# Kernel optimization log

Hardware: AMD Instinct MI355X
Metric: run time of the kernel (lower is better)

The kernel has to match this reference:

```python
import jax, jax.numpy as jnp
import numpy as np

B, S, IN, D, H, L, T, C = 64, 448, 128, 512, 8, 6, 3, 3
FF = 6 * D
MAXLEN = 500
PH = 4  # pooling heads


def _ln(x, w, b, eps=1e-5):
    m = x.mean(-1, keepdims=True)
    v = ((x - m) ** 2).mean(-1, keepdims=True)
    return (x - m) / jnp.sqrt(v + eps) * w + b


def _gelu(x):
    return jax.nn.gelu(x, approximate=False)


def setup_inputs():
    key = jax.random.key(0)
    ks = iter(jax.random.split(key, 64))
    p = lambda *sh: jax.random.normal(next(ks), sh, jnp.float32) * 0.02
    z = lambda *sh: jnp.zeros(sh, jnp.float32)
    o = lambda *sh: jnp.ones(sh, jnp.float32)
    return dict(
        x=jax.random.normal(next(ks), (B, S, IN), jnp.float32),
        in_w1=p(IN, D // 2), in_b1=z(D // 2), in_w2=p(D // 2, D), in_b2=z(D),
        in_ln_w=o(D), in_ln_b=z(D), pos=p(MAXLEN, D), cls=p(1, 1, D),
        wq=p(L, D, D), bq=z(L, D), wk=p(L, D, D), bk=z(L, D),
        wv=p(L, D, D), bv=z(L, D), wo=p(L, D, D), bo=z(L, D),
        conv_w=p(L, D, 1, 3), conv_b=z(L, D), aln_w=o(L, D), aln_b=z(L, D),
        f_w1=p(L, D, FF), f_b1=z(L, FF), f_w2=p(L, FF, FF), f_b2=z(L, FF),
        f_w3=p(L, FF, D), f_b3=z(L, D), g_w=p(L, D, D), g_b=z(L, D),
        n1_w=o(L, D), n1_b=z(L, D), n2_w=o(L, D), n2_b=z(L, D),
        pq=p(1, 1, D), pqw=p(D, D), pqb=z(D), pkw=p(D, D), pkb=z(D),
        pvw=p(D, D), pvb=z(D), pow_w=p(D, D), pow_b=z(D),
        pln_w=o(D), pln_b=z(D),
        h_ln_w=o(T, 2 * D), h_ln_b=z(T, 2 * D),
        h_w1=p(T, 2 * D, 2 * D), h_b1=z(T, 2 * D),
        h_w2=p(T, 2 * D, D), h_b2=z(T, D),
        h_w3=p(T, D, D // 2), h_b3=z(T, D // 2),
        h_w4=p(T, D // 2, C), h_b4=z(T, C),
        u_w1=p(T, 2 * D, D // 2), u_b1=z(T, D // 2),
        u_w2=p(T, D // 2, 1), u_b2=z(T, 1),
    )


def _forward(x, in_w1, in_b1, in_w2, in_b2, in_ln_w, in_ln_b, pos, cls,
             wq, bq, wk, bk, wv, bv, wo, bo, conv_w, conv_b, aln_w, aln_b,
             f_w1, f_b1, f_w2, f_b2, f_w3, f_b3, g_w, g_b,
             n1_w, n1_b, n2_w, n2_b,
             pq, pqw, pqb, pkw, pkb, pvw, pvb, pow_w, pow_b, pln_w, pln_b,
             h_ln_w, h_ln_b, h_w1, h_b1, h_w2, h_b2, h_w3, h_b3, h_w4, h_b4,
             u_w1, u_b1, u_w2, u_b2):
    b = x.shape[0]
    # input projection + norm + pos + cls token
    h = _gelu(x @ in_w1 + in_b1) @ in_w2 + in_b2
    h = _ln(h, in_ln_w, in_ln_b)
    h = h + pos[: h.shape[1]][None]
    h = jnp.concatenate([jnp.broadcast_to(cls, (b, 1, D)), h], axis=1)
    S1 = h.shape[1]  # S + 1
    dk = D // H
    for i in range(L):
        # multi-scale attention (dropout off in eval)
        q = (h @ wq[i] + bq[i]).reshape(b, S1, H, dk)
        k = (h @ wk[i] + bk[i]).reshape(b, S1, H, dk)
        v = (h @ wv[i] + bv[i]).reshape(b, S1, H, dk)
        attn = jax.nn.softmax(jnp.einsum('bqhd,bkhd->bhqk', q, k) / np.sqrt(dk), axis=-1)
        ga = jnp.einsum('bhqk,bkhd->bqhd', attn, v).reshape(b, S1, D) @ wo[i] + bo[i]
        # parallel depthwise conv branch (kernel=3, groups=D)
        la = jax.lax.conv_general_dilated(
            h.transpose(0, 2, 1), conv_w[i], (1,), [(1, 1)],
            dimension_numbers=('NCH', 'OIH', 'NCH'), feature_group_count=D)
        la = (la + conv_b[i][None, :, None]).transpose(0, 2, 1)
        attn_out = _ln(h + (ga + 0.3 * la), aln_w[i], aln_b[i])
        h = _ln(h + attn_out, n1_w[i], n1_b[i])
        # gated FFN
        f = _gelu(h @ f_w1[i] + f_b1[i])
        f = _gelu(f @ f_w2[i] + f_b2[i])
        f = f @ f_w3[i] + f_b3[i]
        gate = jax.nn.sigmoid(h @ g_w[i] + g_b[i])
        h = _ln(h + f * gate, n2_w[i], n2_b[i])
    cls_out = h[:, 0]
    xs = h[:, 1:]
    # attention pooling (torch MHA with 4 heads, single learned query)
    pdk = D // PH
    q = (jnp.broadcast_to(pq, (b, 1, D)) @ pqw + pqb).reshape(b, 1, PH, pdk)
    k = (xs @ pkw + pkb).reshape(b, -1, PH, pdk)
    v = (xs @ pvw + pvb).reshape(b, -1, PH, pdk)
    a = jax.nn.softmax(jnp.einsum('bqhd,bkhd->bhqk', q, k) / np.sqrt(pdk), axis=-1)
    po = jnp.einsum('bhqk,bkhd->bqhd', a, v).reshape(b, 1, D) @ pow_w + pow_b
    pooled = _ln(po[:, 0], pln_w, pln_b)
    comb = jnp.concatenate([cls_out, pooled], axis=-1)  # (B, 2D)
    logits, unc = [], []
    for t in range(T):
        hh = _ln(comb, h_ln_w[t], h_ln_b[t])
        hh = _gelu(hh @ h_w1[t] + h_b1[t])
        hh = _gelu(hh @ h_w2[t] + h_b2[t])
        hh = _gelu(hh @ h_w3[t] + h_b3[t])
        logits.append(hh @ h_w4[t] + h_b4[t])
        uu = jax.nn.relu(comb @ u_w1[t] + u_b1[t]) @ u_w2[t] + u_b2[t]
        unc.append(jax.nn.softplus(uu[:, 0]))
    return jnp.stack(logits, 1), jnp.stack(unc, 1)


def reference(x, in_w1, in_b1, in_w2, in_b2, in_ln_w, in_ln_b, pos, cls,
              wq, bq, wk, bk, wv, bv, wo, bo, conv_w, conv_b, aln_w, aln_b,
              f_w1, f_b1, f_w2, f_b2, f_w3, f_b3, g_w, g_b,
              n1_w, n1_b, n2_w, n2_b,
              pq, pqw, pqb, pkw, pkb, pvw, pvb, pow_w, pow_b, pln_w, pln_b,
              h_ln_w, h_ln_b, h_w1, h_b1, h_w2, h_b2, h_w3, h_b3, h_w4, h_b4,
              u_w1, u_b1, u_w2, u_b2):
    return _forward(x, in_w1, in_b1, in_w2, in_b2, in_ln_w, in_ln_b, pos, cls,
                    wq, bq, wk, bk, wv, bv, wo, bo, conv_w, conv_b, aln_w, aln_b,
                    f_w1, f_b1, f_w2, f_b2, f_w3, f_b3, g_w, g_b,
                    n1_w, n1_b, n2_w, n2_b,
                    pq, pqw, pqb, pkw, pkb, pvw, pvb, pow_w, pow_b, pln_w, pln_b,
                    h_ln_w, h_ln_b, h_w1, h_b1, h_w2, h_b2, h_w3, h_b3, h_w4, h_b4,
                    u_w1, u_b1, u_w2, u_b2)
```

## Files before the change

### kernel.cpp

```cpp
#include <hip/hip_runtime.h>

#define BB 64
#define SS 448
#define S1 449
#define DD 512
#define HH 8
#define LL 6
#define TT 3
#define FF 3072
#define NS 28672
#define N1 28736
#define N1P 28800
#define FBROWS 3712

typedef unsigned short u16;
typedef __attribute__((ext_vector_type(8))) short short8;
typedef __attribute__((ext_vector_type(4))) float floatx4;

#define AS1C(p) ((const __attribute__((address_space(1))) void*)(p))
#define AS3P(p) ((__attribute__((address_space(3))) void*)(p))

__device__ __forceinline__ float b2f(u16 u){
  union { float f; unsigned u; } x; x.u = ((unsigned)u) << 16; return x.f;
}
__device__ __forceinline__ u16 f2b(float f){
  union { float f; unsigned u; } x; x.f = f;
  unsigned r = x.u + 0x7FFFu + ((x.u >> 16) & 1u);
  return (u16)(r >> 16);
}
__device__ __forceinline__ float gelu_f(float v){ return 0.5f*v*(1.f+erff(v*0.70710678118654752440f)); }
__device__ __forceinline__ float sigm_f(float v){ return 1.f/(1.f+expf(-v)); }

__device__ __forceinline__ void reduce2(float& a, float& b, float* scr){
  #pragma unroll
  for (int off=1; off<64; off<<=1){ a += __shfl_xor(a, off); b += __shfl_xor(b, off); }
  const int w = threadIdx.x >> 6;
  __syncthreads();
  if ((threadIdx.x & 63) == 0){ scr[w] = a; scr[4+w] = b; }
  __syncthreads();
  a = scr[0]+scr[1]+scr[2]+scr[3];
  b = scr[4]+scr[5]+scr[6]+scr[7];
}

__global__ void transcvt(const float* __restrict__ src, u16* __restrict__ dst, int K, int N){
  __shared__ float t[32][33];
  const size_t bo = (size_t)blockIdx.z * K * N;
  src += bo; dst += bo;
  const int k0 = blockIdx.x*32, n0 = blockIdx.y*32;
  const int tx = threadIdx.x, ty = threadIdx.y;
  #pragma unroll
  for (int i=0;i<32;i+=8) t[ty+i][tx] = src[(size_t)(k0+ty+i)*N + n0+tx];
  __syncthreads();
  #pragma unroll
  for (int i=0;i<32;i+=8) dst[(size_t)(n0+ty+i)*K + k0+tx] = f2b(t[tx][ty+i]);
}

__global__ void cvt(const float* __restrict__ src, u16* __restrict__ dst, int n){
  int i = blockIdx.x*256 + threadIdx.x;
  if (i < n) dst[i] = f2b(src[i]);
}

template<int ACT, int HASMUL>
__launch_bounds__(256)
__global__ void gemm128(const u16* __restrict__ A, int lda,
                        const u16* __restrict__ Bt, int ldb,
                        const float* __restrict__ bias,
                        u16* __restrict__ Cp, int ldc,
                        const u16* __restrict__ mulp,
                        int K)
{
  __shared__ u16 Al[4096];
  __shared__ u16 Bl[4096];
  const int tid = threadIdx.x;
  const int lane = tid & 63;
  const int w = tid >> 6;
  const int wm = (w >> 1) * 64;
  const int wn = (w & 1) * 64;
  const size_t m0 = (size_t)blockIdx.x * 128;
  const size_t n0 = (size_t)blockIdx.y * 128;

  const int c1 = 256 + tid;
  const u16* a0 = A + (m0 + (tid>>2))*lda + (tid&3)*8;
  const u16* a1 = A + (m0 + (c1>>2))*lda + (c1&3)*8;
  const u16* b0 = Bt + (n0 + (tid>>2))*ldb + (tid&3)*8;
  const u16* b1 = Bt + (n0 + (c1>>2))*ldb + (c1&3)*8;

  const floatx4 fz = {0.f,0.f,0.f,0.f};
  floatx4 acc[4][4];
  #pragma unroll
  for (int i=0;i<4;i++)
    #pragma unroll
    for (int j=0;j<4;j++) acc[i][j] = fz;

  const int fr = lane & 15;
  const int fq = (lane >> 4) * 8;

  for (int k0 = 0; k0 < K; k0 += 32) {
    __syncthreads();
    __builtin_amdgcn_global_load_lds(AS1C(a0), AS3P(Al + w*512),        16, 0, 0);
    __builtin_amdgcn_global_load_lds(AS1C(a1), AS3P(Al + 2048 + w*512), 16, 0, 0);
    __builtin_amdgcn_global_load_lds(AS1C(b0), AS3P(Bl + w*512),        16, 0, 0);
    __builtin_amdgcn_global_load_lds(AS1C(b1), AS3P(Bl + 2048 + w*512), 16, 0, 0);
    a0 += 32; a1 += 32; b0 += 32; b1 += 32;
    __syncthreads();
    short8 af[4], bf[4];
    #pragma unroll
    for (int i=0;i<4;i++) af[i] = *(const short8*)(Al + (wm + i*16 + fr)*32 + fq);
    #pragma unroll
    for (int j=0;j<4;j++) bf[j] = *(const short8*)(Bl + (wn + j*16 + fr)*32 + fq);
    #pragma unroll
    for (int i=0;i<4;i++)
      #pragma unroll
      for (int j=0;j<4;j++)
        acc[i][j] = __builtin_amdgcn_mfma_f32_16x16x32_bf16(af[i], bf[j], acc[i][j], 0, 0, 0);
  }

  const int cr = (lane >> 4) * 4;
  const int cc = lane & 15;
  #pragma unroll
  for (int i=0;i<4;i++) {
    #pragma unroll
    for (int j=0;j<4;j++) {
      const size_t gc = n0 + wn + j*16 + cc;
      const float bv = bias[gc];
      #pragma unroll
      for (int r=0;r<4;r++) {
        const size_t gr = m0 + wm + i*16 + cr + r;
        float vv = acc[i][j][r] + bv;
        if (ACT==1) vv = gelu_f(vv);
        if (ACT==2) vv = sigm_f(vv);
        if (HASMUL) vv *= b2f(mulp[gr*ldc + gc]);
        Cp[gr*ldc + gc] = f2b(vv);
      }
    }
  }
}

__launch_bounds__(256)
__global__ void flash_attn(const u16* __restrict__ qg, const u16* __restrict__ kg,
                           const u16* __restrict__ vg, u16* __restrict__ ctx)
{
  const int bid = blockIdx.x;
  const int qt = bid & 7;
  const int h  = (bid >> 3) & 7;
  const int b  = bid >> 6;
  const int tid = threadIdx.x;
  const int lane = tid & 63;
  const int w = tid >> 6;

  __shared__ u16 Kl[32*64];
  __shared__ u16 Vt[64*72];
  __shared__ u16 Pl[4][16*32];

  const int fr = lane & 15;
  const int fq = (lane >> 4) * 8;

  const int qrow = qt*64 + w*16;
  const size_t qoff = ((size_t)b*S1 + qrow + fr)*DD + h*64 + fq;
  const short8 qf0 = *(const short8*)(qg + qoff);
  const short8 qf1 = *(const short8*)(qg + qoff + 32);

  const floatx4 fz = {0.f,0.f,0.f,0.f};
  floatx4 oacc[4] = {fz, fz, fz, fz};
  float mm[4] = {-3e30f,-3e30f,-3e30f,-3e30f};
  float ll[4] = {0.f,0.f,0.f,0.f};

  const int key_t = tid >> 3;
  const int kch  = tid & 7;
  const u16* gk_base = kg + ((size_t)b*S1 + key_t)*DD + h*64 + kch*8;
  const u16* gv_base = vg + ((size_t)b*S1 + key_t)*DD + h*64 + kch*8;

  for (int k0 = 0; k0 < 480; k0 += 32) {
    __syncthreads();
    __builtin_amdgcn_global_load_lds(AS1C(gk_base + (size_t)k0*DD), AS3P(Kl + w*512), 16, 0, 0);
    {
      short8 tv = *(const short8*)(gv_base + (size_t)k0*DD);
      #pragma unroll
      for (int i=0;i<8;i++) Vt[(kch*8+i)*72 + key_t] = (u16)tv[i];
    }
    __syncthreads();

    floatx4 s0 = fz, s1 = fz;
    {
      short8 kb0  = *(const short8*)(Kl + (size_t)fr*64 + fq);
      short8 kb0h = *(const short8*)(Kl + (size_t)fr*64 + 32 + fq);
      s0 = __builtin_amdgcn_mfma_f32_16x16x32_bf16(qf0, kb0,  s0, 0,0,0);
      s0 = __builtin_amdgcn_mfma_f32_16x16x32_bf16(qf1, kb0h, s0, 0,0,0);
      short8 kb1  = *(const short8*)(Kl + (size_t)(16+fr)*64 + fq);
      short8 kb1h = *(const short8*)(Kl + (size_t)(16+fr)*64 + 32 + fq);
      s1 = __builtin_amdgcn_mfma_f32_16x16x32_bf16(qf0, kb1,  s1, 0,0,0);
      s1 = __builtin_amdgcn_mfma_f32_16x16x32_bf16(qf1, kb1h, s1, 0,0,0);
    }
    const bool msk0 = (k0 + fr) >= S1;
    const bool msk1 = (k0 + 16 + fr) >= S1;
    float p0[4], p1[4];
    #pragma unroll
    for (int r=0;r<4;r++) {
      p0[r] = msk0 ? -3e30f : s0[r]*0.125f;
      p1[r] = msk1 ? -3e30f : s1[r]*0.125f;
    }
    #pragma unroll
    for (int r=0;r<4;r++) {
      float t = fmaxf(p0[r], p1[r]);
      t = fmaxf(t, __shfl_xor(t,1)); t = fmaxf(t, __shfl_xor(t,2));
      t = fmaxf(t, __shfl_xor(t,4)); t = fmaxf(t, __shfl_xor(t,8));
      float mn = fmaxf(mm[r], t);
      float al = __expf(mm[r]-mn);
      mm[r] = mn;
      float e0 = msk0 ? 0.f : __expf(p0[r]-mn);
      float e1 = msk1 ? 0.f : __expf(p1[r]-mn);
      p0[r]=e0; p1[r]=e1;
      float rs = e0+e1;
      rs += __shfl_xor(rs,1); rs += __shfl_xor(rs,2);
      rs += __shfl_xor(rs,4); rs += __shfl_xor(rs,8);
      ll[r] = ll[r]*al + rs;
      oacc[0][r]*=al; oacc[1][r]*=al; oacc[2][r]*=al; oacc[3][r]*=al;
    }
    const int pr = (lane>>4)*4;
    #pragma unroll
    for (int r=0;r<4;r++) {
      Pl[w][(pr+r)*32 + fr]      = f2b(p0[r]);
      Pl[w][(pr+r)*32 + 16 + fr] = f2b(p1[r]);
    }
    short8 pf = *(const short8*)(&Pl[w][fr*32 + fq]);
    #pragma unroll
    for (int j=0;j<4;j++) {
      short8 vb = *(const short8*)(Vt + (size_t)(j*16+fr)*72 + fq);
      oacc[j] = __builtin_amdgcn_mfma_f32_16x16x32_bf16(pf, vb, oacc[j], 0,0,0);
    }
  }
  const int pr = (lane>>4)*4;
  #pragma unroll
  for (int r=0;r<4;r++) {
    const int qi = qrow + pr + r;
    if (qi < S1) {
      const size_t base = ((size_t)b*S1 + qi)*DD + h*64 + fr;
      const float inv = 1.f/ll[r];
      ctx[base]    = f2b(oacc[0][r]*inv);
      ctx[base+16] = f2b(oacc[1][r]*inv);
      ctx[base+32] = f2b(oacc[2][r]*inv);
      ctx[base+48] = f2b(oacc[3][r]*inv);
    }
  }
}

__global__ void ln_pos_cls(const u16* __restrict__ t2, const float* __restrict__ lw,
                           const float* __restrict__ lb, const float* __restrict__ pos,
                           const float* __restrict__ cls, u16* __restrict__ h16)
{
  __shared__ float scr[8];
  const int row = blockIdx.x;
  const int b = row / S1, s = row % S1;
  const int tid = threadIdx.x;
  if (s == 0) {
// ... 111 lines not shown
  __syncthreads();
  mx = fmaxf(fmaxf(scr[0],scr[1]), fmaxf(scr[2],scr[3]));
  float ps = 0.f;
  #pragma unroll
  for (int it=0;it<2;it++){
    const int key = tid+it*256;
    if (key<448) { float p = __expf(s[it]-mx); sc[key]=p; ps += p; }
  }
  #pragma unroll
  for (int off=1; off<64; off<<=1) ps += __shfl_xor(ps, off);
  __syncthreads();
  if ((tid&63)==0) scr[4+w] = ps;
  __syncthreads();
  const float lsum = scr[4]+scr[5]+scr[6]+scr[7];
  const int d = tid & 127, half = tid >> 7;
  float acc = 0.f;
  for (int key = half*224; key < half*224+224; key++)
    acc += sc[key] * b2f(vp[((size_t)b*SS+key)*DD + ph*128 + d]);
  red[tid] = acc;
  __syncthreads();
  if (tid < 128) po[(size_t)b*DD + ph*128 + tid] = f2b((red[tid]+red[tid+128])/lsum);
}

__global__ void comb_build(const u16* __restrict__ hfin, const float* __restrict__ po2,
                           const float* __restrict__ plw, const float* __restrict__ plb,
                           float* __restrict__ c32, u16* __restrict__ c16)
{
  __shared__ float scr[8];
  const int b = blockIdx.x, tid = threadIdx.x;
  #pragma unroll
  for (int e=0;e<2;e++) {
    const int d = tid+e*256;
    const float v = b2f(hfin[((size_t)b*S1)*DD + d]);
    c32[(size_t)b*1024+d] = v; c16[(size_t)b*1024+d] = f2b(v);
  }
  const float* x = po2 + (size_t)b*DD;
  float v0=x[tid], v1=x[tid+256];
  float sa=v0+v1, sb=v0*v0+v1*v1;
  reduce2(sa,sb,scr);
  float mean=sa*(1.f/512.f), var=sb*(1.f/512.f)-mean*mean;
  float inv=rsqrtf(var+1e-5f);
  float r0=(v0-mean)*inv*plw[tid]+plb[tid];
  float r1=(v1-mean)*inv*plw[tid+256]+plb[tid+256];
  c32[(size_t)b*1024+512+tid]=r0; c32[(size_t)b*1024+512+tid+256]=r1;
  c16[(size_t)b*1024+512+tid]=f2b(r0); c16[(size_t)b*1024+512+tid+256]=f2b(r1);
}

__global__ void head_ln(const float* __restrict__ c32, const float* __restrict__ lw,
                        const float* __restrict__ lb, u16* __restrict__ out)
{
  __shared__ float scr[8];
  const int r = blockIdx.x;
  const int t = r / 64, b = r % 64;
  const int tid = threadIdx.x;
  const float* x = c32 + (size_t)b*1024;
  float v[4]; float sa=0.f, sb=0.f;
  #pragma unroll
  for (int e=0;e<4;e++){ v[e]=x[tid+e*256]; sa+=v[e]; sb+=v[e]*v[e]; }
  reduce2(sa,sb,scr);
  float mean=sa*(1.f/1024.f), var=sb*(1.f/1024.f)-mean*mean;
  float inv=rsqrtf(var+1e-5f);
  #pragma unroll
  for (int e=0;e<4;e++){
    const int d = tid+e*256;
    out[(size_t)r*1024+d] = f2b((v[e]-mean)*inv*lw[t*1024+d] + lb[t*1024+d]);
  }
}

template<int ACT, int OUTBF>
__launch_bounds__(256)
__global__ void wavedot(const u16* __restrict__ A, int K, int aMod,
                        const u16* __restrict__ Wt,
                        const float* __restrict__ bias,
                        void* __restrict__ out, int N, int rows, int rowsPerT)
{
  const int gw = (int)(((size_t)blockIdx.x*256 + threadIdx.x) >> 6);
  const int lane = threadIdx.x & 63;
  if (gw >= rows*N) return;
  const int row = gw / N, col = gw % N;
  const int t = row / rowsPerT;
  const int arow = row % aMod;
  const u16* a  = A + (size_t)arow*K;
  const u16* wv = Wt + ((size_t)t*N + col)*K;
  float acc = 0.f;
  for (int k = lane*8; k < K; k += 512) {
    short8 a8 = *(const short8*)(a+k);
    short8 w8 = *(const short8*)(wv+k);
    #pragma unroll
    for (int i=0;i<8;i++) acc += b2f((u16)a8[i]) * b2f((u16)w8[i]);
  }
  #pragma unroll
  for (int off=1; off<64; off<<=1) acc += __shfl_xor(acc, off);
  if (lane == 0) {
    float v = acc + bias[t*N + col];
    if (ACT==1) v = gelu_f(v);
    if (ACT==2) v = fmaxf(v, 0.f);
    if (OUTBF) ((u16*)out)[(size_t)row*N+col] = f2b(v);
    else       ((float*)out)[(size_t)row*N+col] = v;
  }
}

__global__ void logits_k(const float* __restrict__ hh3, const float* __restrict__ w4,
                         const float* __restrict__ b4, float* __restrict__ out)
{
  const int e = blockIdx.x*256 + threadIdx.x;
  if (e >= 576) return;
  const int t = e / 192;
  const int rem = e % 192;
  const int b = rem / 3, c = rem % 3;
  const float* a = hh3 + (size_t)(t*64 + b)*256;
  const float* w = w4 + (size_t)t*256*3 + c;
  float acc = b4[t*3+c];
  for (int k=0;k<256;k++) acc += a[k]*w[k*3];
  out[(size_t)(b*3 + t)*3 + c] = acc;
}

__global__ void u2_k(const float* __restrict__ uu, const float* __restrict__ w2,
                     const float* __restrict__ b2, float* __restrict__ out)
{
  const int e = blockIdx.x*256 + threadIdx.x;
  if (e >= 192) return;
  const int t = e / 64, b = e % 64;
  const float* a = uu + (size_t)e*256;
  const float* w = w2 + (size_t)t*256;
  float acc = b2[t];
  for (int k=0;k<256;k++) acc += a[k]*w[k];
  acc = (acc > 30.f) ? acc : log1pf(expf(acc));
  out[576 + b*3 + t] = acc;
}

extern "C" void kernel_launch(void* const* d_in, const int* in_sizes, int n_in,
                              void* d_out, int out_size, void* d_ws, size_t ws_size,
                              hipStream_t stream)
{
  const float* x      = (const float*)d_in[0];
  const float* in_w1  = (const float*)d_in[1];
  const float* in_b1  = (const float*)d_in[2];
  const float* in_w2  = (const float*)d_in[3];
  const float* in_b2  = (const float*)d_in[4];
  const float* in_lnw = (const float*)d_in[5];
  const float* in_lnb = (const float*)d_in[6];
  const float* pos    = (const float*)d_in[7];
  const float* cls    = (const float*)d_in[8];
  const float* wq     = (const float*)d_in[9];
  const float* bq     = (const float*)d_in[10];
  const float* wk     = (const float*)d_in[11];
  const float* bk     = (const float*)d_in[12];
  const float* wv     = (const float*)d_in[13];
  const float* bv     = (const float*)d_in[14];
// ... 32 lines not shown
  const float* h_b1   = (const float*)d_in[47];
  const float* h_w2   = (const float*)d_in[48];
  const float* h_b2   = (const float*)d_in[49];
  const float* h_w3   = (const float*)d_in[50];
  const float* h_b3   = (const float*)d_in[51];
  const float* h_w4   = (const float*)d_in[52];
  const float* h_b4   = (const float*)d_in[53];
  const float* u_w1   = (const float*)d_in[54];
  const float* u_b1   = (const float*)d_in[55];
  const float* u_w2   = (const float*)d_in[56];
  const float* u_b2   = (const float*)d_in[57];
  float* out = (float*)d_out;

  char* wsp = (char*)d_ws;
  size_t off = 0;
  auto alloc = [&](size_t bytes) -> char* {
    char* p = wsp + off;
    off += (bytes + 255) & ~(size_t)255;
    return p;
  };

  u16* w_in1T = (u16*)alloc((size_t)256*128*2);
  u16* w_in2T = (u16*)alloc((size_t)512*256*2);
  u16* wqT  = (u16*)alloc((size_t)LL*512*512*2);
  u16* wkT  = (u16*)alloc((size_t)LL*512*512*2);
  u16* wvT  = (u16*)alloc((size_t)LL*512*512*2);
  u16* woT  = (u16*)alloc((size_t)LL*512*512*2);
  u16* gwT  = (u16*)alloc((size_t)LL*512*512*2);
  u16* fw1T = (u16*)alloc((size_t)3072*512*2);
  u16* fw2T = (u16*)alloc((size_t)3072*3072*2);
  u16* fw3T = (u16*)alloc((size_t)512*3072*2);
  u16* pkwT = (u16*)alloc((size_t)512*512*2);
  u16* pvwT = (u16*)alloc((size_t)512*512*2);
  u16* powT = (u16*)alloc((size_t)512*512*2);
  u16* pqwT = (u16*)alloc((size_t)512*512*2);
  u16* hw1T = (u16*)alloc((size_t)TT*1024*1024*2);
  u16* hw2T = (u16*)alloc((size_t)TT*512*1024*2);
  u16* hw3T = (u16*)alloc((size_t)TT*256*512*2);
  u16* uw1T = (u16*)alloc((size_t)TT*256*1024*2);

  u16* hA16 = (u16*)alloc((size_t)N1P*DD*2);
  u16* hB16 = (u16*)alloc((size_t)N1P*DD*2);
  u16* q16  = (u16*)alloc((size_t)N1P*DD*2);
  u16* k16  = (u16*)alloc((size_t)N1P*DD*2);
  u16* v16  = (u16*)alloc((size_t)N1P*DD*2);
  u16* fbuf1 = (u16*)alloc((size_t)FBROWS*FF*2);
  u16* fbuf2 = (u16*)alloc((size_t)FBROWS*FF*2);
  u16* ctx16  = hB16;
  u16* tmpa16 = k16;
  u16* gate16 = q16;
  u16* x16 = fbuf1;
  u16* t1b = fbuf2;
  u16* pq16   = (u16*)alloc(512*2);
  float* qvec = (float*)alloc(512*4);
  u16* po16   = (u16*)alloc((size_t)64*512*2);
  float* po2  = (float*)alloc((size_t)64*512*4);
  float* comb32 = (float*)alloc((size_t)64*1024*4);
  u16*   comb16 = (u16*)alloc((size_t)64*1024*2);
  u16* hh0 = (u16*)alloc((size_t)192*1024*2);
  u16* hh1 = (u16*)alloc((size_t)192*1024*2);
  u16* hh2 = (u16*)alloc((size_t)192*512*2);
  float* hh3 = (float*)alloc((size_t)192*256*4);
  float* uu  = (float*)alloc((size_t)192*256*4);
  (void)ws_size;

  const dim3 tb(32,8);
  transcvt<<<dim3(4,8,1),   tb, 0, stream>>>(in_w1, w_in1T, 128, 256);
  transcvt<<<dim3(8,16,1),  tb, 0, stream>>>(in_w2, w_in2T, 256, 512);
  transcvt<<<dim3(16,16,LL),tb, 0, stream>>>(wq,  wqT, 512, 512);
  transcvt<<<dim3(16,16,LL),tb, 0, stream>>>(wk,  wkT, 512, 512);
  transcvt<<<dim3(16,16,LL),tb, 0, stream>>>(wv,  wvT, 512, 512);
  transcvt<<<dim3(16,16,LL),tb, 0, stream>>>(wo,  woT, 512, 512);
  transcvt<<<dim3(16,16,LL),tb, 0, stream>>>(g_w, gwT, 512, 512);
  transcvt<<<dim3(16,16,1), tb, 0, stream>>>(pkw,   pkwT, 512, 512);
  transcvt<<<dim3(16,16,1), tb, 0, stream>>>(pvw,   pvwT, 512, 512);
  transcvt<<<dim3(16,16,1), tb, 0, stream>>>(pow_w, powT, 512, 512);
  transcvt<<<dim3(16,16,1), tb, 0, stream>>>(pqw,   pqwT, 512, 512);
  transcvt<<<dim3(32,32,TT),tb, 0, stream>>>(h_w1, hw1T, 1024, 1024);
  transcvt<<<dim3(32,16,TT),tb, 0, stream>>>(h_w2, hw2T, 1024, 512);
  transcvt<<<dim3(16,8,TT), tb, 0, stream>>>(h_w3, hw3T, 512, 256);
  transcvt<<<dim3(32,8,TT), tb, 0, stream>>>(u_w1, uw1T, 1024, 256);

  cvt<<<(NS*128+255)/256, 256, 0, stream>>>(x,  x16,  NS*128);
  cvt<<<2, 256, 0, stream>>>(pqv, pq16, 512);

  gemm128<1,0><<<dim3(224,2),256,0,stream>>>(x16,128, w_in1T,128, in_b1, t1b,256, nullptr, 128);
  gemm128<0,0><<<dim3(224,4),256,0,stream>>>(t1b,256, w_in2T,256, in_b2, tmpa16,512, nullptr, 256);
  ln_pos_cls<<<N1,256,0,stream>>>(tmpa16, in_lnw, in_lnb, pos, cls, hA16);

  static const int CH_T[8] = {29,28,28,28,28,28,28,28};

  for (int i=0;i<LL;i++){
    const size_t wOff = (size_t)i*512*512;
    transcvt<<<dim3(16,96,1),tb,0,stream>>>(f_w1 + (size_t)i*512*3072,  fw1T, 512, 3072);
    transcvt<<<dim3(96,96,1),tb,0,stream>>>(f_w2 + (size_t)i*3072*3072, fw2T, 3072, 3072);
    transcvt<<<dim3(96,16,1),tb,0,stream>>>(f_w3 + (size_t)i*3072*512,  fw3T, 3072, 512);

    gemm128<0,0><<<dim3(225,4),256,0,stream>>>(hA16,512, wqT+wOff,512, bq+i*512, q16,512, nullptr, 512);
    gemm128<0,0><<<dim3(225,4),256,0,stream>>>(hA16,512, wkT+wOff,512, bk+i*512, k16,512, nullptr, 512);
    gemm128<0,0><<<dim3(225,4),256,0,stream>>>(hA16,512, wvT+wOff,512, bv+i*512, v16,512, nullptr, 512);
    flash_attn<<<4096,256,0,stream>>>(q16,k16,v16,ctx16);
    gemm128<0,0><<<dim3(225,4),256,0,stream>>>(ctx16,512, woT+wOff,512, bo+i*512, tmpa16,512, nullptr, 512);
    attn_merge<<<N1,256,0,stream>>>(hA16, tmpa16, conv_w+(size_t)i*1536, conv_b+i*512,
                                    aln_w+i*512, aln_b+i*512, n1_w+i*512, n1_b+i*512, hB16);
    gemm128<2,0><<<dim3(225,4),256,0,stream>>>(hB16,512, gwT+wOff,512, g_b+i*512, gate16,512, nullptr, 512);
    int t0 = 0;
    for (int c=0;c<8;c++){
      const int nt = CH_T[c];
      const size_t r0 = (size_t)t0*128;
      gemm128<1,0><<<dim3(nt,24),256,0,stream>>>(hB16 + r0*512, 512, fw1T, 512, f_b1+i*3072, fbuf1, 3072, nullptr, 512);
      gemm128<1,0><<<dim3(nt,24),256,0,stream>>>(fbuf1, 3072, fw2T, 3072, f_b2+i*3072, fbuf2, 3072, nullptr, 3072);
      gemm128<0,1><<<dim3(nt,4), 256,0,stream>>>(fbuf2, 3072, fw3T, 3072, f_b3+i*512, tmpa16 + r0*512, 512, gate16 + r0*512, 3072);
      t0 += nt;
    }
    resid_ln<<<N1,256,0,stream>>>(hB16, tmpa16, n2_w+i*512, n2_b+i*512, hA16);
  }

  xs_compact<<<NS*64/256,256,0,stream>>>(hA16, q16);
  gemm128<0,0><<<dim3(224,4),256,0,stream>>>(q16,512, pkwT,512, pkb, k16,512, nullptr, 512);
  gemm128<0,0><<<dim3(224,4),256,0,stream>>>(q16,512, pvwT,512, pvb, v16,512, nullptr, 512);
  wavedot<0,0><<<128,256,0,stream>>>(pq16, 512, 1, pqwT, pqb, qvec, 512, 1, 1);
  pool_attn<<<256,256,0,stream>>>(qvec, k16, v16, po16);
  wavedot<0,0><<<8192,256,0,stream>>>(po16, 512, 64, powT, pow_b, po2, 512, 64, 64);
  comb_build<<<64,256,0,stream>>>(hA16, po2, pln_w, pln_b, comb32, comb16);

  head_ln<<<192,256,0,stream>>>(comb32, h_lnw, h_lnb, hh0);
  wavedot<1,1><<<49152,256,0,stream>>>(hh0, 1024, 192, hw1T, h_b1, hh1, 1024, 192, 64);
  wavedot<1,1><<<24576,256,0,stream>>>(hh1, 1024, 192, hw2T, h_b2, hh2, 512, 192, 64);
  wavedot<1,0><<<12288,256,0,stream>>>(hh2, 512, 192, hw3T, h_b3, hh3, 256, 192, 64);
  logits_k<<<3,256,0,stream>>>(hh3, h_w4, h_b4, out);
  wavedot<2,0><<<12288,256,0,stream>>>(comb16, 1024, 64, uw1T, u_b1, uu, 256, 192, 64);
  u2_k<<<1,256,0,stream>>>(uu, u_w2, u_b2, out);
}
```

Measured before the change: 12.86 ms.

## Fuse Q/K projections, pre-transpose V for attention, and move heads to MFMA GEMMs

Q and K weights are concatenated so one GEMM produces an interleaved QK buffer. V is transposed by a separate kernel so flash attention can load it straight into LDS with swizzled layouts, and the P tile padding changes. The FFN third GEMM runs once over all rows when workspace allows, and the pooling output projection and classification/uncertainty heads move from per-wave dot products to batched MFMA GEMMs padded to 128 rows per task. This trades launch count, LDS bank conflicts and scalar dot-product work for extra buffers, an extra transpose pass, and padded rows.

New measurement: 10.43 ms. -18.9%, faster.

```diff
diff --git a/kernel.cpp b/kernel.cpp
--- a/kernel.cpp
+++ b/kernel.cpp
@@ -11,7 +11,7 @@
 #define NS 28672
 #define N1 28736
 #define N1P 28800
-#define FBROWS 3712
+#define FB1 ((size_t)3712*3072)
 
 typedef unsigned short u16;
 typedef __attribute__((ext_vector_type(8))) short short8;
@@ -42,10 +42,10 @@
   b = scr[4]+scr[5]+scr[6]+scr[7];
 }
 
-__global__ void transcvt(const float* __restrict__ src, u16* __restrict__ dst, int K, int N){
+__global__ void transcvt(const float* __restrict__ src, u16* __restrict__ dst, int K, int N, size_t dls){
   __shared__ float t[32][33];
-  const size_t bo = (size_t)blockIdx.z * K * N;
-  src += bo; dst += bo;
+  src += (size_t)blockIdx.z * K * N;
+  dst += (size_t)blockIdx.z * dls;
   const int k0 = blockIdx.x*32, n0 = blockIdx.y*32;
   const int tx = threadIdx.x, ty = threadIdx.y;
   #pragma unroll
@@ -60,7 +60,14 @@
   if (i < n) dst[i] = f2b(src[i]);
 }
 
-template<int ACT, int HASMUL>
+__global__ void biascat(const float* __restrict__ a, const float* __restrict__ b, float* __restrict__ dst){
+  int i = blockIdx.x*256 + threadIdx.x;
+  if (i >= LL*1024) return;
+  int l = i >> 10, c = i & 1023;
+  dst[i] = (c < 512) ? a[l*512 + c] : b[l*512 + (c-512)];
+}
+
+template<int ACT, int HASMUL, int TSEL>
 __launch_bounds__(256)
 __global__ void gemm128(const u16* __restrict__ A, int lda,
                         const u16* __restrict__ Bt, int ldb,
@@ -78,12 +85,18 @@
   const int wn = (w & 1) * 64;
   const size_t m0 = (size_t)blockIdx.x * 128;
   const size_t n0 = (size_t)blockIdx.y * 128;
+  if (TSEL) {
+    const int N = gridDim.y * 128;
+    Bt  += (size_t)blockIdx.x * N * ldb;
+    bias += (size_t)blockIdx.x * N;
+  }
 
   const int c1 = 256 + tid;
   const u16* a0 = A + (m0 + (tid>>2))*lda + (tid&3)*8;
   const u16* a1 = A + (m0 + (c1>>2))*lda + (c1&3)*8;
-  const u16* b0 = Bt + (n0 + (tid>>2))*ldb + (tid&3)*8;
-  const u16* b1 = Bt + (n0 + (c1>>2))*ldb + (c1&3)*8;
+  const u16* b0 = Bt + ((TSEL?0:n0) + (tid>>2))*ldb + (tid&3)*8;
+  const u16* b1 = Bt + ((TSEL?0:n0) + (c1>>2))*ldb + (c1&3)*8;
+  if (TSEL) { b0 += n0*ldb; b1 += n0*ldb; }
 
   const floatx4 fz = {0.f,0.f,0.f,0.f};
   floatx4 acc[4][4];
@@ -122,13 +135,14 @@
     #pragma unroll
     for (int j=0;j<4;j++) {
       const size_t gc = n0 + wn + j*16 + cc;
-      const float bv = bias[gc];
+      const float bv = bias[gc - (TSEL ? 0 : 0)];
       #pragma unroll
       for (int r=0;r<4;r++) {
         const size_t gr = m0 + wm + i*16 + cr + r;
         float vv = acc[i][j][r] + bv;
         if (ACT==1) vv = gelu_f(vv);
         if (ACT==2) vv = sigm_f(vv);
+        if (ACT==3) vv = fmaxf(vv, 0.f);
         if (HASMUL) vv *= b2f(mulp[gr*ldc + gc]);
         Cp[gr*ldc + gc] = f2b(vv);
       }
@@ -136,9 +150,31 @@
   }
 }
 
+__global__ void vtrans(const u16* __restrict__ v, u16* __restrict__ vT){
+  __shared__ u16 t[32][72];
+  const int bh = blockIdx.y;
+  const int b = bh >> 3, h = bh & 7;
+  const int k0 = blockIdx.x * 32;
+  const int tid = threadIdx.x;
+  {
+    const int key = tid >> 3, dch = tid & 7;
+    const int ka = k0 + key;
+    short8 val = {0,0,0,0,0,0,0,0};
+    if (ka < S1) val = *(const short8*)(v + ((size_t)b*S1 + ka)*DD + h*64 + dch*8);
+    *(short8*)(&t[key][dch*8]) = val;
+  }
+  __syncthreads();
+  const int d = tid >> 2, kk = tid & 3;
+  short8 o;
+  #pragma unroll
+  for (int i=0;i<8;i++) o[i] = (short)t[kk*8+i][d];
+  *(short8*)(vT + ((size_t)bh*64 + d)*512 + k0 + kk*8) = o;
+}
+
 __launch_bounds__(256)
-__global__ void flash_attn(const u16* __restrict__ qg, const u16* __restrict__ kg,
-                           const u16* __restrict__ vg, u16* __restrict__ ctx)
+__global__ void flash_attn(const u16* __restrict__ qkg,
+                           const u16* __restrict__ vT,
+                           u16* __restrict__ ctx)
 {
   const int bid = blockIdx.x;
   const int qt = bid & 7;
@@ -148,46 +184,48 @@
   const int lane = tid & 63;
   const int w = tid >> 6;
 
-  __shared__ u16 Kl[32*64];
-  __shared__ u16 Vt[64*72];
-  __shared__ u16 Pl[4][16*32];
+  __shared__ u16 Kl[2048];
+  __shared__ u16 Vl[2048];
+  __shared__ u16 Pl[4][16*40];
 
   const int fr = lane & 15;
-  const int fq = (lane >> 4) * 8;
+  const int q4 = lane >> 4;
+  const int fq = q4 * 8;
 
   const int qrow = qt*64 + w*16;
-  const size_t qoff = ((size_t)b*S1 + qrow + fr)*DD + h*64 + fq;
-  const short8 qf0 = *(const short8*)(qg + qoff);
-  const short8 qf1 = *(const short8*)(qg + qoff + 32);
+  const size_t qoff = ((size_t)b*S1 + qrow + fr)*1024 + h*64 + fq;
+  const short8 qf0 = *(const short8*)(qkg + qoff);
+  const short8 qf1 = *(const short8*)(qkg + qoff + 32);
 
   const floatx4 fz = {0.f,0.f,0.f,0.f};
   floatx4 oacc[4] = {fz, fz, fz, fz};
   float mm[4] = {-3e30f,-3e30f,-3e30f,-3e30f};
   float ll[4] = {0.f,0.f,0.f,0.f};
 
-  const int key_t = tid >> 3;
-  const int kch  = tid & 7;
-  const u16* gk_base = kg + ((size_t)b*S1 + key_t)*DD + h*64 + kch*8;
-  const u16* gv_base = vg + ((size_t)b*S1 + key_t)*DD + h*64 + kch*8;
+  const u16* gk = qkg + ((size_t)b*S1 + (tid>>3))*1024 + 512 + h*64
+                + (((tid&7) ^ ((tid>>3)&7)) * 8);
+  const u16* gv = vT + ((size_t)(b*8+h)*64 + (tid>>2))*512
+                + (((tid&3) ^ ((tid>>2)&3)) * 8);
+
+  const int kswz0 = (( q4      ^ (fr&7)) * 8);
+  const int kswz1 = (((4+q4)   ^ (fr&7)) * 8);
+  const int vswz  = (( q4      ^ (fr&3)) * 8);
 
   for (int k0 = 0; k0 < 480; k0 += 32) {
     __syncthreads();
-    __builtin_amdgcn_global_load_lds(AS1C(gk_base + (size_t)k0*DD), AS3P(Kl + w*512), 16, 0, 0);
-    {
-      short8 tv = *(const short8*)(gv_base + (size_t)k0*DD);
-      #pragma unroll
-      for (int i=0;i<8;i++) Vt[(kch*8+i)*72 + key_t] = (u16)tv[i];
-    }
+    __builtin_amdgcn_global_load_lds(AS1C(gk), AS3P(Kl + w*512), 16, 0, 0);
+    __builtin_amdgcn_global_load_lds(AS1C(gv), AS3P(Vl + w*512), 16, 0, 0);
+    gk += 32*1024; gv += 32;
     __syncthreads();
 
     floatx4 s0 = fz, s1 = fz;
     {
-      short8 kb0  = *(const short8*)(Kl + (size_t)fr*64 + fq);
-      short8 kb0h = *(const short8*)(Kl + (size_t)fr*64 + 32 + fq);
+      short8 kb0  = *(const short8*)(Kl + fr*64 + kswz0);
+      short8 kb0h = *(const short8*)(Kl + fr*64 + kswz1);
       s0 = __builtin_amdgcn_mfma_f32_16x16x32_bf16(qf0, kb0,  s0, 0,0,0);
       s0 = __builtin_amdgcn_mfma_f32_16x16x32_bf16(qf1, kb0h, s0, 0,0,0);
-      short8 kb1  = *(const short8*)(Kl + (size_t)(16+fr)*64 + fq);
-      short8 kb1h = *(const short8*)(Kl + (size_t)(16+fr)*64 + 32 + fq);
+      short8 kb1  = *(const short8*)(Kl + (16+fr)*64 + kswz0);
+      short8 kb1h = *(const short8*)(Kl + (16+fr)*64 + kswz1);
       s1 = __builtin_amdgcn_mfma_f32_16x16x32_bf16(qf0, kb1,  s1, 0,0,0);
       s1 = __builtin_amdgcn_mfma_f32_16x16x32_bf16(qf1, kb1h, s1, 0,0,0);
     }
@@ -216,20 +254,20 @@
       ll[r] = ll[r]*al + rs;
       oacc[0][r]*=al; oacc[1][r]*=al; oacc[2][r]*=al; oacc[3][r]*=al;
     }
-    const int pr = (lane>>4)*4;
+    const int pr = q4*4;
     #pragma unroll
     for (int r=0;r<4;r++) {
-      Pl[w][(pr+r)*32 + fr]      = f2b(p0[r]);
-      Pl[w][(pr+r)*32 + 16 + fr] = f2b(p1[r]);
-    }
-    short8 pf = *(const short8*)(&Pl[w][fr*32 + fq]);
+      Pl[w][(pr+r)*40 + fr]      = f2b(p0[r]);
+      Pl[w][(pr+r)*40 + 16 + fr] = f2b(p1[r]);
+    }
+    short8 pf = *(const short8*)(&Pl[w][fr*40 + fq]);
     #pragma unroll
     for (int j=0;j<4;j++) {
-      short8 vb = *(const short8*)(Vt + (size_t)(j*16+fr)*72 + fq);
+      short8 vb = *(const short8*)(Vl + (j*16+fr)*32 + vswz);
       oacc[j] = __builtin_amdgcn_mfma_f32_16x16x32_bf16(pf, vb, oacc[j], 0,0,0);
     }
   }
-  const int pr = (lane>>4)*4;
+  const int pr = q4*4;
   #pragma unroll
   for (int r=0;r<4;r++) {
     const int qi = qrow + pr + r;
@@ -387,69 +425,65 @@
   if (tid < 128) po[(size_t)b*DD + ph*128 + tid] = f2b((red[tid]+red[tid+128])/lsum);
 }
 
-__global__ void comb_build(const u16* __restrict__ hfin, const float* __restrict__ po2,
+__global__ void comb_build(const u16* __restrict__ hfin, const u16* __restrict__ po2,
                            const float* __restrict__ plw, const float* __restrict__ plb,
-                           float* __restrict__ c32, u16* __restrict__ c16)
+                           u16* __restrict__ c384)
 {
   __shared__ float scr[8];
   const int b = blockIdx.x, tid = threadIdx.x;
-  #pragma unroll
-  for (int e=0;e<2;e++) {
-    const int d = tid+e*256;
-    const float v = b2f(hfin[((size_t)b*S1)*DD + d]);
-    c32[(size_t)b*1024+d] = v; c16[(size_t)b*1024+d] = f2b(v);
-  }
-  const float* x = po2 + (size_t)b*DD;
-  float v0=x[tid], v1=x[tid+256];
+  const u16 c0 = hfin[((size_t)b*S1)*DD + tid];
+  const u16 c1 = hfin[((size_t)b*S1)*DD + tid + 256];
+  float v0 = b2f(po2[(size_t)b*DD + tid]);
+  float v1 = b2f(po2[(size_t)b*DD + tid + 256]);
   float sa=v0+v1, sb=v0*v0+v1*v1;
   reduce2(sa,sb,scr);
   float mean=sa*(1.f/512.f), var=sb*(1.f/512.f)-mean*mean;
   float inv=rsqrtf(var+1e-5f);
-  float r0=(v0-mean)*inv*plw[tid]+plb[tid];
-  float r1=(v1-mean)*inv*plw[tid+256]+plb[tid+256];
-  c32[(size_t)b*1024+512+tid]=r0; c32[(size_t)b*1024+512+tid+256]=r1;
-  c16[(size_t)b*1024+512+tid]=f2b(r0); c16[(size_t)b*1024+512+tid+256]=f2b(r1);
-}
-
-__global__ void head_ln(const float* __restrict__ c32, const float* __restrict__ lw,
+  u16 r0=f2b((v0-mean)*inv*plw[tid]+plb[tid]);
+  u16 r1=f2b((v1-mean)*inv*plw[tid+256]+plb[tid+256]);
+  #pragma unroll
+  for (int t=0;t<3;t++){
+    const size_t base = (size_t)(t*128+b)*1024;
+    c384[base+tid]=c0; c384[base+tid+256]=c1;
+    c384[base+512+tid]=r0; c384[base+512+tid+256]=r1;
+  }
+}
+
+__global__ void head_ln(const u16* __restrict__ comb, const float* __restrict__ lw,
                         const float* __restrict__ lb, u16* __restrict__ out)
 {
   __shared__ float scr[8];
   const int r = blockIdx.x;
   const int t = r / 64, b = r % 64;
   const int tid = threadIdx.x;
-  const float* x = c32 + (size_t)b*1024;
+  const u16* x = comb + (size_t)b*1024;
   float v[4]; float sa=0.f, sb=0.f;
   #pragma unroll
-  for (int e=0;e<4;e++){ v[e]=x[tid+e*256]; sa+=v[e]; sb+=v[e]*v[e]; }
+  for (int e=0;e<4;e++){ v[e]=b2f(x[tid+e*256]); sa+=v[e]; sb+=v[e]*v[e]; }
   reduce2(sa,sb,scr);
   float mean=sa*(1.f/1024.f), var=sb*(1.f/1024.f)-mean*mean;
   float inv=rsqrtf(var+1e-5f);
   #pragma unroll
   for (int e=0;e<4;e++){
     const int d = tid+e*256;
-    out[(size_t)r*1024+d] = f2b((v[e]-mean)*inv*lw[t*1024+d] + lb[t*1024+d]);
-  }
-}
-
-template<int ACT, int OUTBF>
+    out[(size_t)(t*128+b)*1024+d] = f2b((v[e]-mean)*inv*lw[t*1024+d] + lb[t*1024+d]);
+  }
+}
+
+template<int ACT>
 __launch_bounds__(256)
-__global__ void wavedot(const u16* __restrict__ A, int K, int aMod,
+__global__ void wavedot(const u16* __restrict__ A, int K,
                         const u16* __restrict__ Wt,
                         const float* __restrict__ bias,
-                        void* __restrict__ out, int N, int rows, int rowsPerT)
+                        float* __restrict__ out, int N)
 {
   const int gw = (int)(((size_t)blockIdx.x*256 + threadIdx.x) >> 6);
   const int lane = threadIdx.x & 63;
-  if (gw >= rows*N) return;
-  const int row = gw / N, col = gw % N;
-  const int t = row / rowsPerT;
-  const int arow = row % aMod;
-  const u16* a  = A + (size_t)arow*K;
-  const u16* wv = Wt + ((size_t)t*N + col)*K;
+  if (gw >= N) return;
+  const u16* wv = Wt + (size_t)gw*K;
   float acc = 0.f;
   for (int k = lane*8; k < K; k += 512) {
-    short8 a8 = *(const short8*)(a+k);
+    short8 a8 = *(const short8*)(A+k);
     short8 w8 = *(const short8*)(wv+k);
     #pragma unroll
     for (int i=0;i<8;i++) acc += b2f((u16)a8[i]) * b2f((u16)w8[i]);
@@ -457,15 +491,13 @@
   #pragma unroll
   for (int off=1; off<64; off<<=1) acc += __shfl_xor(acc, off);
   if (lane == 0) {
-    float v = acc + bias[t*N + col];
+    float v = acc + bias[gw];
     if (ACT==1) v = gelu_f(v);
-    if (ACT==2) v = fmaxf(v, 0.f);
-    if (OUTBF) ((u16*)out)[(size_t)row*N+col] = f2b(v);
-    else       ((float*)out)[(size_t)row*N+col] = v;
-  }
-}
-
-__global__ void logits_k(const float* __restrict__ hh3, const float* __restrict__ w4,
+    out[gw] = v;
+  }
+}
+
+__global__ void logits_k(const u16* __restrict__ hh3, const float* __restrict__ w4,
                          const float* __restrict__ b4, float* __restrict__ out)
 {
   const int e = blockIdx.x*256 + threadIdx.x;
@@ -473,23 +505,24 @@
   const int t = e / 192;
   const int rem = e % 192;
   const int b = rem / 3, c = rem % 3;
-  const float* a = hh3 + (size_t)(t*64 + b)*256;
+  const u16* a = hh3 + (size_t)(t*128 + b)*256;
   const float* w = w4 + (size_t)t*256*3 + c;
   float acc = b4[t*3+c];
-  for (int k=0;k<256;k++) acc += a[k]*w[k*3];
+  for (int k=0;k<256;k++) acc += b2f(a[k])*w[k*3];
   out[(size_t)(b*3 + t)*3 + c] = acc;
 }
 
-__global__ void u2_k(const float* __restrict__ uu, const float* __restrict__ w2,
-                     const float* __restrict__ b2, float* __restrict__ out)
+__global__ void u2_k(const float* __restrict__ , const u16* __restrict__ uu,
+                     const float* __restrict__ w2, const float* __restrict__ b2,
+                     float* __restrict__ out)
 {
   const int e = blockIdx.x*256 + threadIdx.x;
   if (e >= 192) return;
   const int t = e / 64, b = e % 64;
-  const float* a = uu + (size_t)e*256;
+  const u16* a = uu + (size_t)(t*128 + b)*256;
   const float* w = w2 + (size_t)t*256;
   float acc = b2[t];
-  for (int k=0;k<256;k++) acc += a[k]*w[k];
+  for (int k=0;k<256;k++) acc += b2f(a[k])*w[k];
   acc = (acc > 30.f) ? acc : log1pf(expf(acc));
   out[576 + b*3 + t] = acc;
 }
@@ -568,8 +601,7 @@
 
   u16* w_in1T = (u16*)alloc((size_t)256*128*2);
   u16* w_in2T = (u16*)alloc((size_t)512*256*2);
-  u16* wqT  = (u16*)alloc((size_t)LL*512*512*2);
-  u16* wkT  = (u16*)alloc((size_t)LL*512*512*2);
+  u16* qkT  = (u16*)alloc((size_t)LL*1024*512*2);
   u16* wvT  = (u16*)alloc((size_t)LL*512*512*2);
   u16* woT  = (u16*)alloc((size_t)LL*512*512*2);
   u16* gwT  = (u16*)alloc((size_t)LL*512*512*2);
@@ -584,97 +616,132 @@
   u16* hw2T = (u16*)alloc((size_t)TT*512*1024*2);
   u16* hw3T = (u16*)alloc((size_t)TT*256*512*2);
   u16* uw1T = (u16*)alloc((size_t)TT*256*1024*2);
-
-  u16* hA16 = (u16*)alloc((size_t)N1P*DD*2);
+  float* bqk = (float*)alloc((size_t)LL*1024*4);
+
   u16* hB16 = (u16*)alloc((size_t)N1P*DD*2);
-  u16* q16  = (u16*)alloc((size_t)N1P*DD*2);
-  u16* k16  = (u16*)alloc((size_t)N1P*DD*2);
-  u16* v16  = (u16*)alloc((size_t)N1P*DD*2);
-  u16* fbuf1 = (u16*)alloc((size_t)FBROWS*FF*2);
-  u16* fbuf2 = (u16*)alloc((size_t)FBROWS*FF*2);
-  u16* ctx16  = hB16;
-  u16* tmpa16 = k16;
-  u16* gate16 = q16;
-  u16* x16 = fbuf1;
-  u16* t1b = fbuf2;
+  u16* qk16 = (u16*)alloc((size_t)N1P*1024*2);
+  u16* gate16 = qk16;
+  u16* tmp16  = qk16 + (size_t)N1P*512;
   u16* pq16   = (u16*)alloc(512*2);
   float* qvec = (float*)alloc(512*4);
-  u16* po16   = (u16*)alloc((size_t)64*512*2);
-  float* po2  = (float*)alloc((size_t)64*512*4);
-  float* comb32 = (float*)alloc((size_t)64*1024*4);
-  u16*   comb16 = (u16*)alloc((size_t)64*1024*2);
-  u16* hh0 = (u16*)alloc((size_t)192*1024*2);
-  u16* hh1 = (u16*)alloc((size_t)192*1024*2);
-  u16* hh2 = (u16*)alloc((size_t)192*512*2);
-  float* hh3 = (float*)alloc((size_t)192*256*4);
-  float* uu  = (float*)alloc((size_t)192*256*4);
-  (void)ws_size;
+  u16* po16   = (u16*)alloc((size_t)128*512*2);
+  u16* po2bf  = (u16*)alloc((size_t)128*512*2);
+  u16* c384   = (u16*)alloc((size_t)384*1024*2);
+  u16* hh0 = (u16*)alloc((size_t)384*1024*2);
+  u16* hh1 = (u16*)alloc((size_t)384*1024*2);
+  u16* hh2 = (u16*)alloc((size_t)384*512*2);
+  u16* hh3 = (u16*)alloc((size_t)384*256*2);
+  u16* uu  = (u16*)alloc((size_t)384*256*2);
+
+  const size_t off_common = off;
+  size_t off_big;
+  u16 *fbuf1_b, *v16_b, *hA16_b, *fbuf2_b, *vT_b;
+  {
+    off = off_common;
+    fbuf1_b = (u16*)alloc(FB1*2);
+    v16_b   = (u16*)alloc((size_t)N1P*512*2);
+    hA16_b  = (u16*)alloc((size_t)N1P*512*2);
+    alloc((size_t)N1P*2048*2);
+    fbuf2_b = v16_b;
+    vT_b    = fbuf2_b + (size_t)N1P*1024;
+    off_big = off;
+  }
+  u16 *fbuf1_s, *fbuf2_s, *v16_s, *hA16_s, *vT_s;
+  {
+    off = off_common;
+    fbuf1_s = (u16*)alloc(FB1*2);
+    fbuf2_s = (u16*)alloc(FB1*2);
+    v16_s   = (u16*)alloc((size_t)N1P*512*2);
+    hA16_s  = (u16*)alloc((size_t)N1P*512*2);
+    vT_s    = fbuf1_s;
+  }
+  const bool big = ws_size >= off_big;
+  u16* fbuf1 = big ? fbuf1_b : fbuf1_s;
+  u16* fbuf2 = big ? fbuf2_b : fbuf2_s;
+  u16* v16   = big ? v16_b   : v16_s;
+  u16* hA16  = big ? hA16_b  : hA16_s;
+  u16* vT    = big ? vT_b    : vT_s;
+  u16* x16 = fbuf1;
+  u16* t1b = fbuf1 + 3670016;
 
   const dim3 tb(32,8);
-  transcvt<<<dim3(4,8,1),   tb, 0, stream>>>(in_w1, w_in1T, 128, 256);
-  transcvt<<<dim3(8,16,1),  tb, 0, stream>>>(in_w2, w_in2T, 256, 512);
-  transcvt<<<dim3(16,16,LL),tb, 0, stream>>>(wq,  wqT, 512, 512);
-  transcvt<<<dim3(16,16,LL),tb, 0, stream>>>(wk,  wkT, 512, 512);
-  transcvt<<<dim3(16,16,LL),tb, 0, stream>>>(wv,  wvT, 512, 512);
-  transcvt<<<dim3(16,16,LL),tb, 0, stream>>>(wo,  woT, 512, 512);
-  transcvt<<<dim3(16,16,LL),tb, 0, stream>>>(g_w, gwT, 512, 512);
-  transcvt<<<dim3(16,16,1), tb, 0, stream>>>(pkw,   pkwT, 512, 512);
-  transcvt<<<dim3(16,16,1), tb, 0, stream>>>(pvw,   pvwT, 512, 512);
-  transcvt<<<dim3(16,16,1), tb, 0, stream>>>(pow_w, powT, 512, 512);
-  transcvt<<<dim3(16,16,1), tb, 0, stream>>>(pqw,   pqwT, 512, 512);
-  transcvt<<<dim3(32,32,TT),tb, 0, stream>>>(h_w1, hw1T, 1024, 1024);
-  transcvt<<<dim3(32,16,TT),tb, 0, stream>>>(h_w2, hw2T, 1024, 512);
-  transcvt<<<dim3(16,8,TT), tb, 0, stream>>>(h_w3, hw3T, 512, 256);
-  transcvt<<<dim3(32,8,TT), tb, 0, stream>>>(u_w1, uw1T, 1024, 256);
+  transcvt<<<dim3(4,8,1),   tb, 0, stream>>>(in_w1, w_in1T, 128, 256, 0);
+  transcvt<<<dim3(8,16,1),  tb, 0, stream>>>(in_w2, w_in2T, 256, 512, 0);
+  transcvt<<<dim3(16,16,LL),tb, 0, stream>>>(wq,  qkT,             512, 512, (size_t)1024*512);
+  transcvt<<<dim3(16,16,LL),tb, 0, stream>>>(wk,  qkT + 512*512,   512, 512, (size_t)1024*512);
+  transcvt<<<dim3(16,16,LL),tb, 0, stream>>>(wv,  wvT, 512, 512, (size_t)512*512);
+  transcvt<<<dim3(16,16,LL),tb, 0, stream>>>(wo,  woT, 512, 512, (size_t)512*512);
+  transcvt<<<dim3(16,16,LL),tb, 0, stream>>>(g_w, gwT, 512, 512, (size_t)512*512);
+  transcvt<<<dim3(16,16,1), tb, 0, stream>>>(pkw,   pkwT, 512, 512, 0);
+  transcvt<<<dim3(16,16,1), tb, 0, stream>>>(pvw,   pvwT, 512, 512, 0);
+  transcvt<<<dim3(16,16,1), tb, 0, stream>>>(pow_w, powT, 512, 512, 0);
+  transcvt<<<dim3(16,16,1), tb, 0, stream>>>(pqw,   pqwT, 512, 512, 0);
+  transcvt<<<dim3(32,32,TT),tb, 0, stream>>>(h_w1, hw1T, 1024, 1024, (size_t)1024*1024);
+  transcvt<<<dim3(32,16,TT),tb, 0, stream>>>(h_w2, hw2T, 1024, 512, (size_t)512*1024);
+  transcvt<<<dim3(16,8,TT), tb, 0, stream>>>(h_w3, hw3T, 512, 256, (size_t)256*512);
+  transcvt<<<dim3(32,8,TT), tb, 0, stream>>>(u_w1, uw1T, 1024, 256, (size_t)256*1024);
+  biascat<<<24,256,0,stream>>>(bq, bk, bqk);
 
   cvt<<<(NS*128+255)/256, 256, 0, stream>>>(x,  x16,  NS*128);
   cvt<<<2, 256, 0, stream>>>(pqv, pq16, 512);
 
-  gemm128<1,0><<<dim3(224,2),256,0,stream>>>(x16,128, w_in1T,128, in_b1, t1b,256, nullptr, 128);
-  gemm128<0,0><<<dim3(224,4),256,0,stream>>>(t1b,256, w_in2T,256, in_b2, tmpa16,512, nullptr, 256);
-  ln_pos_cls<<<N1,256,0,stream>>>(tmpa16, in_lnw, in_lnb, pos, cls, hA16);
+  gemm128<1,0,0><<<dim3(224,2),256,0,stream>>>(x16,128, w_in1T,128, in_b1, t1b,256, nullptr, 128);
+  gemm128<0,0,0><<<dim3(224,4),256,0,stream>>>(t1b,256, w_in2T,256, in_b2, tmp16,512, nullptr, 256);
+  ln_pos_cls<<<N1,256,0,stream>>>(tmp16, in_lnw, in_lnb, pos, cls, hA16);
 
   static const int CH_T[8] = {29,28,28,28,28,28,28,28};
 
   for (int i=0;i<LL;i++){
     const size_t wOff = (size_t)i*512*512;
-    transcvt<<<dim3(16,96,1),tb,0,stream>>>(f_w1 + (size_t)i*512*3072,  fw1T, 512, 3072);
-    transcvt<<<dim3(96,96,1),tb,0,stream>>>(f_w2 + (size_t)i*3072*3072, fw2T, 3072, 3072);
-    transcvt<<<dim3(96,16,1),tb,0,stream>>>(f_w3 + (size_t)i*3072*512,  fw3T, 3072, 512);
-
-    gemm128<0,0><<<dim3(225,4),256,0,stream>>>(hA16,512, wqT+wOff,512, bq+i*512, q16,512, nullptr, 512);
-    gemm128<0,0><<<dim3(225,4),256,0,stream>>>(hA16,512, wkT+wOff,512, bk+i*512, k16,512, nullptr, 512);
-    gemm128<0,0><<<dim3(225,4),256,0,stream>>>(hA16,512, wvT+wOff,512, bv+i*512, v16,512, nullptr, 512);
-    flash_attn<<<4096,256,0,stream>>>(q16,k16,v16,ctx16);
-    gemm128<0,0><<<dim3(225,4),256,0,stream>>>(ctx16,512, woT+wOff,512, bo+i*512, tmpa16,512, nullptr, 512);
-    attn_merge<<<N1,256,0,stream>>>(hA16, tmpa16, conv_w+(size_t)i*1536, conv_b+i*512,
+    transcvt<<<dim3(16,96,1),tb,0,stream>>>(f_w1 + (size_t)i*512*3072,  fw1T, 512, 3072, 0);
+    transcvt<<<dim3(96,96,1),tb,0,stream>>>(f_w2 + (size_t)i*3072*3072, fw2T, 3072, 3072, 0);
+    transcvt<<<dim3(96,16,1),tb,0,stream>>>(f_w3 + (size_t)i*3072*512,  fw3T, 3072, 512, 0);
+
+    gemm128<0,0,0><<<dim3(225,8),256,0,stream>>>(hA16,512, qkT+(size_t)i*1024*512,512, bqk+i*1024, qk16,1024, nullptr, 512);
+    gemm128<0,0,0><<<dim3(225,4),256,0,stream>>>(hA16,512, wvT+wOff,512, bv+i*512, v16,512, nullptr, 512);
+    vtrans<<<dim3(15,512),256,0,stream>>>(v16, vT);
+    flash_attn<<<4096,256,0,stream>>>(qk16, vT, hB16);
+    gemm128<0,0,0><<<dim3(225,4),256,0,stream>>>(hB16,512, woT+wOff,512, bo+i*512, tmp16,512, nullptr, 512);
+    attn_merge<<<N1,256,0,stream>>>(hA16, tmp16, conv_w+(size_t)i*1536, conv_b+i*512,
                                     aln_w+i*512, aln_b+i*512, n1_w+i*512, n1_b+i*512, hB16);
-    gemm128<2,0><<<dim3(225,4),256,0,stream>>>(hB16,512, gwT+wOff,512, g_b+i*512, gate16,512, nullptr, 512);
-    int t0 = 0;
-    for (int c=0;c<8;c++){
-      const int nt = CH_T[c];
-      const size_t r0 = (size_t)t0*128;
-      gemm128<1,0><<<dim3(nt,24),256,0,stream>>>(hB16 + r0*512, 512, fw1T, 512, f_b1+i*3072, fbuf1, 3072, nullptr, 512);
-      gemm128<1,0><<<dim3(nt,24),256,0,stream>>>(fbuf1, 3072, fw2T, 3072, f_b2+i*3072, fbuf2, 3072, nullptr, 3072);
-      gemm128<0,1><<<dim3(nt,4), 256,0,stream>>>(fbuf2, 3072, fw3T, 3072, f_b3+i*512, tmpa16 + r0*512, 512, gate16 + r0*512, 3072);
-      t0 += nt;
-    }
-    resid_ln<<<N1,256,0,stream>>>(hB16, tmpa16, n2_w+i*512, n2_b+i*512, hA16);
-  }
-
-  xs_compact<<<NS*64/256,256,0,stream>>>(hA16, q16);
-  gemm128<0,0><<<dim3(224,4),256,0,stream>>>(q16,512, pkwT,512, pkb, k16,512, nullptr, 512);
-  gemm128<0,0><<<dim3(224,4),256,0,stream>>>(q16,512, pvwT,512, pvb, v16,512, nullptr, 512);
-  wavedot<0,0><<<128,256,0,stream>>>(pq16, 512, 1, pqwT, pqb, qvec, 512, 1, 1);
-  pool_attn<<<256,256,0,stream>>>(qvec, k16, v16, po16);
-  wavedot<0,0><<<8192,256,0,stream>>>(po16, 512, 64, powT, pow_b, po2, 512, 64, 64);
-  comb_build<<<64,256,0,stream>>>(hA16, po2, pln_w, pln_b, comb32, comb16);
-
-  head_ln<<<192,256,0,stream>>>(comb32, h_lnw, h_lnb, hh0);
-  wavedot<1,1><<<49152,256,0,stream>>>(hh0, 1024, 192, hw1T, h_b1, hh1, 1024, 192, 64);
-  wavedot<1,1><<<24576,256,0,stream>>>(hh1, 1024, 192, hw2T, h_b2, hh2, 512, 192, 64);
-  wavedot<1,0><<<12288,256,0,stream>>>(hh2, 512, 192, hw3T, h_b3, hh3, 256, 192, 64);
+    gemm128<2,0,0><<<dim3(225,4),256,0,stream>>>(hB16,512, gwT+wOff,512, g_b+i*512, gate16,512, nullptr, 512);
+    if (big) {
+      int t0 = 0;
+      for (int c=0;c<8;c++){
+        const int nt = CH_T[c];
+        const size_t r0 = (size_t)t0*128;
+        gemm128<1,0,0><<<dim3(nt,24),256,0,stream>>>(hB16 + r0*512, 512, fw1T, 512, f_b1+i*3072, fbuf1, 3072, nullptr, 512);
+        gemm128<1,0,0><<<dim3(nt,24),256,0,stream>>>(fbuf1, 3072, fw2T, 3072, f_b2+i*3072, fbuf2 + r0*3072, 3072, nullptr, 3072);
+        t0 += nt;
+      }
+      gemm128<0,1,0><<<dim3(225,4),256,0,stream>>>(fbuf2, 3072, fw3T, 3072, f_b3+i*512, tmp16, 512, gate16, 3072);
+    } else {
+      int t0 = 0;
+      for (int c=0;c<8;c++){
+        const int nt = CH_T[c];
+        const size_t r0 = (size_t)t0*128;
+        gemm128<1,0,0><<<dim3(nt,24),256,0,stream>>>(hB16 + r0*512, 512, fw1T, 512, f_b1+i*3072, fbuf1, 3072, nullptr, 512);
+        gemm128<1,0,0><<<dim3(nt,24),256,0,stream>>>(fbuf1, 3072, fw2T, 3072, f_b2+i*3072, fbuf2, 3072, nullptr, 3072);
+        gemm128<0,1,0><<<dim3(nt,4), 256,0,stream>>>(fbuf2, 3072, fw3T, 3072, f_b3+i*512, tmp16 + r0*512, 512, gate16 + r0*512, 3072);
+        t0 += nt;
+      }
+    }
+    resid_ln<<<N1,256,0,stream>>>(hB16, tmp16, n2_w+i*512, n2_b+i*512, hA16);
+  }
+
+  xs_compact<<<NS*64/256,256,0,stream>>>(hA16, hB16);
+  gemm128<0,0,0><<<dim3(224,4),256,0,stream>>>(hB16,512, pkwT,512, pkb, gate16,512, nullptr, 512);
+  gemm128<0,0,0><<<dim3(224,4),256,0,stream>>>(hB16,512, pvwT,512, pvb, tmp16,512, nullptr, 512);
+  wavedot<0><<<8,256,0,stream>>>(pq16, 512, pqwT, pqb, qvec, 512);
+  pool_attn<<<256,256,0,stream>>>(qvec, gate16, tmp16, po16);
+  gemm128<0,0,0><<<dim3(1,4),256,0,stream>>>(po16,512, powT,512, pow_b, po2bf,512, nullptr, 512);
+  comb_build<<<64,256,0,stream>>>(hA16, po2bf, pln_w, pln_b, c384);
+
+  head_ln<<<192,256,0,stream>>>(c384, h_lnw, h_lnb, hh0);
+  gemm128<1,0,1><<<dim3(3,8),256,0,stream>>>(hh0,1024, hw1T,1024, h_b1, hh1,1024, nullptr, 1024);
+  gemm128<1,0,1><<<dim3(3,4),256,0,stream>>>(hh1,1024, hw2T,1024, h_b2, hh2,512, nullptr, 1024);
+  gemm128<1,0,1><<<dim3(3,2),256,0,stream>>>(hh2,512,  hw3T,512,  h_b3, hh3,256, nullptr, 512);
   logits_k<<<3,256,0,stream>>>(hh3, h_w4, h_b4, out);
-  wavedot<2,0><<<12288,256,0,stream>>>(comb16, 1024, 64, uw1T, u_b1, uu, 256, 192, 64);
-  u2_k<<<1,256,0,stream>>>(uu, u_w2, u_b2, out);
-}
+  gemm128<3,0,1><<<dim3(3,2),256,0,stream>>>(c384,1024, uw1T,1024, u_b1, uu,256, nullptr, 1024);
+  u2_k<<<1,256,0,stream>>>(nullptr, uu, u_w2, u_b2, out);
+}
```
